# Performance work log

Hardware: AMD Instinct MI355X
Metric: run time of the kernel (lower is better)

The kernel has to match this reference:

```python
import jax, jax.numpy as jnp
import numpy as np

N = 500_000
N_ATOMS = 5
T = 8                # angle triplets per (residue, bead) table row
CONT_LEN = 36
GATE_OFFSET = 1
NUM_EXPERTS = 18
BEAD_COL = 36
MAX_BEADS = 4
ANGLE_WEIGHT = 1.0
EPS = 1e-8
MIN_LEN = 0.02


def setup_inputs() -> dict:
    key = jax.random.key(0)
    ks = jax.random.split(key, 8)
    x = jax.random.uniform(ks[0], (N, 38), dtype=jnp.float32)
    # gate column holds residue id in [1, num_experts]; bead column in [0, max_beads)
    res = jax.random.randint(ks[1], (N,), 1, NUM_EXPERTS + 1).astype(jnp.float32)
    bead = jax.random.randint(ks[2], (N,), 0, MAX_BEADS).astype(jnp.float32)
    x = x.at[:, CONT_LEN + 1].set(res)
    x = x.at[:, BEAD_COL].set(bead)
    y_true = jax.random.normal(ks[3], (N, N_ATOMS * 3), dtype=jnp.float32)
    y_pred = jax.random.normal(ks[4], (N, N_ATOMS * 3), dtype=jnp.float32)
    mask = (jax.random.uniform(ks[5], (N, N_ATOMS * 3)) < 0.85).astype(jnp.float32)
    # -1 entries act as invalid-triplet sentinels (trip_ok branch)
    trip = jax.random.randint(ks[6], (NUM_EXPERTS, MAX_BEADS, T, 3), -1, N_ATOMS, dtype=jnp.int32)
    valid = jax.random.randint(ks[7], (NUM_EXPERTS, MAX_BEADS, T), 0, 2, dtype=jnp.int32)
    return {"x": x, "y_true": y_true, "y_pred": y_pred, "mask": mask,
            "angle_triplets_table": trip, "angle_valid_table": valid}


def _atom_mse(true, pred, m):
    # masked per-atom squared error, normalized by count of valid atoms per sample
    se_atom = jnp.sum(jnp.square(true - pred) * m, axis=-1)          # [N, A]
    atom_valid = jnp.any(m > 0.0, axis=-1).astype(se_atom.dtype)     # [N, A]
    num = jnp.sum(se_atom * atom_valid, axis=-1)
    den = jnp.sum(atom_valid, axis=-1) + EPS
    return jnp.mean(num / den)


def _angle_loss(x, true, pred, m, trip_table, valid_table):
    gate = x[:, CONT_LEN + 1]
    gate = jnp.where(jnp.isfinite(gate), gate, 0.0)
    res_id = jnp.clip(jnp.round(gate).astype(jnp.int32) - GATE_OFFSET, 0, NUM_EXPERTS - 1)
    bead = x[:, BEAD_COL]
    bead = jnp.where(jnp.isfinite(bead), bead, 0.0)
    bead_id = jnp.clip(jnp.round(bead).astype(jnp.int32), 0, MAX_BEADS - 1)

    atom_valid = jnp.any(m > 0.0, axis=-1)                           # [N, A]
    trip = trip_table[res_id, bead_id]                               # [N, T, 3]
    base_valid = valid_table[res_id, bead_id]                        # [N, T]
    trip_ok = jnp.all(trip >= 0, axis=-1)
    ts = jnp.maximum(trip, 0)
    i_idx, j_idx, k_idx = ts[..., 0], ts[..., 1], ts[..., 2]         # [N, T]

    rows = jnp.arange(true.shape[0])[:, None]
    vi = atom_valid[rows, i_idx]
    vj = atom_valid[rows, j_idx]
    vk = atom_valid[rows, k_idx]
    ti, tj, tk = true[rows, i_idx], true[rows, j_idx], true[rows, k_idx]   # [N, T, 3]
    pi, pj, pk = pred[rows, i_idx], pred[rows, j_idx], pred[rows, k_idx]

    v1t, v2t, v1p, v2p = ti - tj, tk - tj, pi - pj, pk - pj
    ml2 = jnp.float32(MIN_LEN * MIN_LEN)
    sq = lambda v: jnp.sum(jnp.square(v), axis=-1)
    l1t2, l2t2, l1p2, l2p2 = sq(v1t), sq(v2t), sq(v1p), sq(v2p)

    valid = (trip_ok & (base_valid > 0) & vi & vj & vk
             & (l1t2 > ml2) & (l2t2 > ml2) & (l1p2 > ml2) & (l2p2 > ml2))

    unit = lambda v, l2: v * jax.lax.rsqrt(jnp.maximum(l2, ml2))[..., None]
    u1t, u2t = unit(v1t, l1t2), unit(v2t, l2t2)
    u1p, u2p = unit(v1p, l1p2), unit(v2p, l2p2)

    clip = lambda c: jnp.clip(c, -1.0 + 1e-6, 1.0 - 1e-6)
    cos_t = clip(jnp.sum(u1t * u2t, axis=-1))
    cos_p = clip(jnp.sum(u1p * u2p, axis=-1))
    sin_t = jnp.linalg.norm(jnp.cross(u1t, u2t), axis=-1)
    sin_p = jnp.linalg.norm(jnp.cross(u1p, u2p), axis=-1)

    per_ang = jnp.square(cos_p - cos_t) + jnp.square(sin_p - sin_t)
    per_ang = jnp.where(valid, per_ang, 0.0)
    num = jnp.sum(per_ang, axis=-1)
    den = jnp.sum(valid.astype(jnp.float32), axis=-1) + EPS
    return jnp.mean(num / den)


def reference(x, y_true, y_pred, mask, angle_triplets_table, angle_valid_table):
    true = y_true.reshape(-1, N_ATOMS, 3).astype(jnp.float32)
    pred = y_pred.reshape(-1, N_ATOMS, 3).astype(jnp.float32)
    m = mask.reshape(-1, N_ATOMS, 3).astype(jnp.float32)
    atom = _atom_mse(true, pred, m)
    ang = _angle_loss(x, true, pred, m, angle_triplets_table, angle_valid_table)
    return atom + ANGLE_WEIGHT * ang
```

## Files before the change

kernel.cpp:

```cpp
#include <hip/hip_runtime.h>
#include <math.h>

#define NEXP 18
#define NBEAD 4
#define EPSV 1e-8f
#define ML2 (0.02f * 0.02f)

#define AS1U(p) ((const __attribute__((address_space(1))) unsigned*)(p))
#define AS3U(p) ((__attribute__((address_space(3))) unsigned*)(p))

__global__ __launch_bounds__(256, 5) void loss_kernel(
    const float* __restrict__ xin, const float* __restrict__ y_true,
    const float* __restrict__ y_pred, const float* __restrict__ mask,
    const int* __restrict__ trip, const int* __restrict__ valid,
    float* __restrict__ partial, int n) {
    __shared__ float sT[3840];
    __shared__ float sP[3840];
    __shared__ unsigned sBits[124];
    __shared__ unsigned sTbl[72][4];

    const int tid = threadIdx.x;
    const int lane = tid & 63;
    const int wv = tid >> 6;

    if (tid < 124) sBits[tid] = 0u;
    if (tid < NEXP * NBEAD) {
        unsigned w[4] = {0u, 0u, 0u, 0u};
#pragma unroll
        for (int t = 0; t < 8; t++) {
            int b = tid * 8 + t;
            int i = trip[b * 3 + 0], j = trip[b * 3 + 1], k = trip[b * 3 + 2];
            unsigned ok = (i >= 0 && j >= 0 && k >= 0 && valid[b] > 0) ? 1u : 0u;
            unsigned oi = 3u * (unsigned)min(max(i, 0), 4);
            unsigned oj = 3u * (unsigned)min(max(j, 0), 4);
            unsigned ov = 3u * (unsigned)min(max(k, 0), 4);
            unsigned e = oi | (oj << 4) | (ov << 8) | (ok << 12);
            w[t >> 1] |= e << ((t & 1) * 16);
        }
        sTbl[tid][0] = w[0]; sTbl[tid][1] = w[1];
        sTbl[tid][2] = w[2]; sTbl[tid][3] = w[3];
    }
    __syncthreads();

    const int row0 = blockIdx.x * 256;
    int rows = n - row0;
    if (rows > 256) rows = 256;
    const int cnt = rows * 15;
    const int cnt4 = cnt >> 2;
    const size_t base = (size_t)row0 * 15;
    const float4* gt = (const float4*)(y_true + base);
    const float4* gp = (const float4*)(y_pred + base);
    const float4* gm = (const float4*)(mask + base);
    float4* sT4 = (float4*)sT;
    float4* sP4 = (float4*)sP;

    for (int ib = wv * 64; ib + 64 <= cnt4; ib += 256) {
        __builtin_amdgcn_global_load_lds(AS1U(gt + ib + lane), AS3U(sT4 + ib), 16, 0, 0);
        __builtin_amdgcn_global_load_lds(AS1U(gp + ib + lane), AS3U(sP4 + ib), 16, 0, 0);
    }
    for (int i = (cnt4 & ~63) + tid; i < cnt4; i += 256) { sT4[i] = gt[i]; sP4[i] = gp[i]; }
    for (int i = (cnt4 << 2) + tid; i < cnt; i += 256) {
        sT[i] = y_true[base + i];
        sP[i] = y_pred[base + i];
    }

    for (int i = tid; i < cnt4; i += 256) {
        float4 m4 = gm[i];
        unsigned b0 = (m4.x > 0.f ? 1u : 0u) | (m4.y > 0.f ? 2u : 0u) |
                      (m4.z > 0.f ? 4u : 0u) | (m4.w > 0.f ? 8u : 0u);
        if (b0) {
            int e = i << 2;
            unsigned long long v = (unsigned long long)b0 << (e & 31);
            atomicOr(&sBits[e >> 5], (unsigned)v);
            unsigned hi = (unsigned)(v >> 32);
            if (hi) atomicOr(&sBits[(e >> 5) + 1], hi);
        }
    }
    for (int i = (cnt4 << 2) + tid; i < cnt; i += 256) {
        if (mask[base + i] > 0.f) atomicOr(&sBits[i >> 5], 1u << (i & 31));
    }
    __syncthreads();

    float result = 0.0f;
    const int row = row0 + tid;
    if (row < n) {
        const float* st = sT + tid * 15;
        const float* sp = sP + tid * 15;
        const int bb = tid * 15;
        unsigned long long mw =
            ((unsigned long long)sBits[(bb >> 5) + 1] << 32) | sBits[bb >> 5];
        const unsigned mrow = (unsigned)((mw >> (bb & 31)) & 0x7fffu);

        float num_a = 0.f, den_a = 0.f;
        unsigned avm2 = 0u;
#pragma unroll
        for (int a = 0; a < 5; a++) {
            unsigned mb = (mrow >> (3 * a)) & 7u;
            float d0 = st[3 * a + 0] - sp[3 * a + 0];
            float d1 = st[3 * a + 1] - sp[3 * a + 1];
            float d2 = st[3 * a + 2] - sp[3 * a + 2];
            float se = (mb & 1u ? d0 * d0 : 0.f) + (mb & 2u ? d1 * d1 : 0.f) +
                       (mb & 4u ? d2 * d2 : 0.f);
            if (mb) { num_a += se; den_a += 1.f; avm2 |= 1u << (3 * a); }
        }
        result = num_a / (den_a + EPSV);

        float2 gb = *(const float2*)(xin + (size_t)row * 38 + 36);
        float beadf = isfinite(gb.x) ? gb.x : 0.f;
        float gatef = isfinite(gb.y) ? gb.y : 0.f;
        gatef = fminf(fmaxf(gatef, -1e6f), 1e6f);
        beadf = fminf(fmaxf(beadf, -1e6f), 1e6f);
        int res_id = min(max((int)rintf(gatef) - 1, 0), NEXP - 1);
        int bead_id = min(max((int)rintf(beadf), 0), NBEAD - 1);
        int combo = res_id * NBEAD + bead_id;
        unsigned tw0 = sTbl[combo][0], tw1 = sTbl[combo][1];
        unsigned tw2 = sTbl[combo][2], tw3 = sTbl[combo][3];

        float num_g = 0.f, den_g = 0.f;
#pragma unroll
        for (int t = 0; t < 8; t++) {
            unsigned wrd = (t < 2) ? tw0 : (t < 4) ? tw1 : (t < 6) ? tw2 : tw3;
            unsigned e = (wrd >> ((t & 1) * 16)) & 0xffffu;
            int oi = e & 15, oj = (e >> 4) & 15, ov = (e >> 8) & 15;
            bool wok = ((e >> 12) & 1u) != 0u;

            float tix = st[oi], tiy = st[oi + 1], tiz = st[oi + 2];
            float tjx = st[oj], tjy = st[oj + 1], tjz = st[oj + 2];
            float tkx = st[ov], tky = st[ov + 1], tkz = st[ov + 2];
            float pix = sp[oi], piy = sp[oi + 1], piz = sp[oi + 2];
            float pjx = sp[oj], pjy = sp[oj + 1], pjz = sp[oj + 2];
            float pkx = sp[ov], pky = sp[ov + 1], pkz = sp[ov + 2];

            float v1tx = tix - tjx, v1ty = tiy - tjy, v1tz = tiz - tjz;
            float v2tx = tkx - tjx, v2ty = tky - tjy, v2tz = tkz - tjz;
            float v1px = pix - pjx, v1py = piy - pjy, v1pz = piz - pjz;
            float v2px = pkx - pjx, v2py = pky - pjy, v2pz = pkz - pjz;

            float l1t = fmaf(v1tx, v1tx, fmaf(v1ty, v1ty, v1tz * v1tz));
            float l2t = fmaf(v2tx, v2tx, fmaf(v2ty, v2ty, v2tz * v2tz));
            float l1p = fmaf(v1px, v1px, fmaf(v1py, v1py, v1pz * v1pz));
            float l2p = fmaf(v2px, v2px, fmaf(v2py, v2py, v2pz * v2pz));

            bool okv = wok && ((avm2 >> oi) & 1) && ((avm2 >> oj) & 1) &&
                       ((avm2 >> ov) & 1) && (l1t > ML2) && (l2t > ML2) &&
                       (l1p > ML2) && (l2p > ML2);

            float rt = __builtin_amdgcn_rsqf(fmaxf(l1t, ML2) * fmaxf(l2t, ML2));
            float rp = __builtin_amdgcn_rsqf(fmaxf(l1p, ML2) * fmaxf(l2p, ML2));

            float dott = fmaf(v1tx, v2tx, fmaf(v1ty, v2ty, v1tz * v2tz));
            float dotp = fmaf(v1px, v2px, fmaf(v1py, v2py, v1pz * v2pz));
            float cut = dott * rt;
            float cup = dotp * rp;
            float cost = fminf(fmaxf(cut, -1.f + 1e-6f), 1.f - 1e-6f);
            float cosp = fminf(fmaxf(cup, -1.f + 1e-6f), 1.f - 1e-6f);
            float sint = __builtin_amdgcn_sqrtf(fmaxf(fmaf(-cut, cut, 1.f), 0.f));
            float sinp = __builtin_amdgcn_sqrtf(fmaxf(fmaf(-cup, cup, 1.f), 0.f));

            float dc = cosp - cost, dsn = sinp - sint;
            if (okv) { num_g += fmaf(dc, dc, dsn * dsn); den_g += 1.f; }
        }
        result += num_g / (den_g + EPSV);
    }

    __syncthreads();
#pragma unroll
    for (int off = 32; off > 0; off >>= 1)
        result += __shfl_down(result, off, 64);
    float* red = (float*)sBits;
    if (lane == 0) red[wv] = result;
    __syncthreads();
    if (tid == 0) partial[blockIdx.x] = red[0] + red[1] + red[2] + red[3];
}

__global__ __launch_bounds__(256) void reduce_kernel(const float* __restrict__ partial,
                                                     float* __restrict__ out, int nblocks,
                                                     float inv_n) {
    __shared__ float red[4];
    float s = 0.f;
    for (int i = threadIdx.x; i < nblocks; i += 256) s += partial[i];
#pragma unroll
    for (int off = 32; off > 0; off >>= 1) s += __shfl_down(s, off, 64);
    int lane = threadIdx.x & 63, wv = threadIdx.x >> 6;
    if (lane == 0) red[wv] = s;
    __syncthreads();
    if (threadIdx.x == 0) out[0] = (red[0] + red[1] + red[2] + red[3]) * inv_n;
}

extern "C" void kernel_launch(void* const* d_in, const int* in_sizes, int n_in,
                              void* d_out, int out_size, void* d_ws, size_t ws_size,
                              hipStream_t stream) {
    const float* x = (const float*)d_in[0];
    const float* y_true = (const float*)d_in[1];
    const float* y_pred = (const float*)d_in[2];
    const float* mask = (const float*)d_in[3];
    const int* trip = (const int*)d_in[4];
    const int* valid = (const int*)d_in[5];
    float* out = (float*)d_out;
    float* partial = (float*)d_ws;

    const int n = in_sizes[1] / 15;
    const int blocks = (n + 255) / 256;

    loss_kernel<<<blocks, 256, 0, stream>>>(x, y_true, y_pred, mask, trip, valid, partial, n);
    reduce_kernel<<<1, 256, 0, stream>>>(partial, out, blocks, 1.0f / (float)n);
}
```

Baseline: 191.1 us.

## Load rows directly per thread, pack triplet table in separate kernel

Drops the cooperative global-to-LDS block staging and the shared-memory mask bitfield built with atomics. Each thread now loads its own 15 true/pred/mask floats straight from global memory into registers and copies them to a private padded LDS slot for indexed gathers. Table packing moves to a one-block pre-kernel that writes to workspace, which removes the start-of-block syncs. The cost is uncoalesced per-thread strided loads (60-byte row stride) and one extra kernel launch.

```diff
diff --git a/kernel.cpp b/kernel.cpp
--- a/kernel.cpp
+++ b/kernel.cpp
@@ -1,109 +1,56 @@
 #include <hip/hip_runtime.h>
 #include <math.h>
 
+#define NATOMS 5
 #define NEXP 18
 #define NBEAD 4
 #define EPSV 1e-8f
 #define ML2 (0.02f * 0.02f)
 
-#define AS1U(p) ((const __attribute__((address_space(1))) unsigned*)(p))
-#define AS3U(p) ((__attribute__((address_space(3))) unsigned*)(p))
+__global__ void pack_tables(const int* __restrict__ trip, const int* __restrict__ valid,
+                            int4* __restrict__ ptbl) {
+    int c = blockIdx.x * blockDim.x + threadIdx.x;
+    if (c < NEXP * NBEAD) {
+        unsigned w[4] = {0u, 0u, 0u, 0u};
+#pragma unroll
+        for (int t = 0; t < 8; t++) {
+            int b = c * 8 + t;
+            int i = trip[b * 3 + 0], j = trip[b * 3 + 1], k = trip[b * 3 + 2];
+            unsigned ok = (i >= 0 && j >= 0 && k >= 0 && valid[b] > 0) ? 1u : 0u;
+            unsigned oi = 3u * (unsigned)min(max(i, 0), NATOMS - 1);
+            unsigned oj = 3u * (unsigned)min(max(j, 0), NATOMS - 1);
+            unsigned ov = 3u * (unsigned)min(max(k, 0), NATOMS - 1);
+            unsigned e = oi | (oj << 4) | (ov << 8) | (ok << 12);
+            w[t >> 1] |= e << ((t & 1) * 16);
+        }
+        ptbl[c] = make_int4((int)w[0], (int)w[1], (int)w[2], (int)w[3]);
+    }
+}
 
 __global__ __launch_bounds__(256, 5) void loss_kernel(
     const float* __restrict__ xin, const float* __restrict__ y_true,
     const float* __restrict__ y_pred, const float* __restrict__ mask,
-    const int* __restrict__ trip, const int* __restrict__ valid,
-    float* __restrict__ partial, int n) {
-    __shared__ float sT[3840];
-    __shared__ float sP[3840];
-    __shared__ unsigned sBits[124];
-    __shared__ unsigned sTbl[72][4];
+    const int4* __restrict__ ptbl, float* __restrict__ partial, int n) {
+    __shared__ float scr[8192];
 
     const int tid = threadIdx.x;
-    const int lane = tid & 63;
-    const int wv = tid >> 6;
-
-    if (tid < 124) sBits[tid] = 0u;
-    if (tid < NEXP * NBEAD) {
-        unsigned w[4] = {0u, 0u, 0u, 0u};
-#pragma unroll
-        for (int t = 0; t < 8; t++) {
-            int b = tid * 8 + t;
-            int i = trip[b * 3 + 0], j = trip[b * 3 + 1], k = trip[b * 3 + 2];
-            unsigned ok = (i >= 0 && j >= 0 && k >= 0 && valid[b] > 0) ? 1u : 0u;
-            unsigned oi = 3u * (unsigned)min(max(i, 0), 4);
-            unsigned oj = 3u * (unsigned)min(max(j, 0), 4);
-            unsigned ov = 3u * (unsigned)min(max(k, 0), 4);
-            unsigned e = oi | (oj << 4) | (ov << 8) | (ok << 12);
-            w[t >> 1] |= e << ((t & 1) * 16);
-        }
-        sTbl[tid][0] = w[0]; sTbl[tid][1] = w[1];
-        sTbl[tid][2] = w[2]; sTbl[tid][3] = w[3];
-    }
-    __syncthreads();
-
-    const int row0 = blockIdx.x * 256;
-    int rows = n - row0;
-    if (rows > 256) rows = 256;
-    const int cnt = rows * 15;
-    const int cnt4 = cnt >> 2;
-    const size_t base = (size_t)row0 * 15;
-    const float4* gt = (const float4*)(y_true + base);
-    const float4* gp = (const float4*)(y_pred + base);
-    const float4* gm = (const float4*)(mask + base);
-    float4* sT4 = (float4*)sT;
-    float4* sP4 = (float4*)sP;
-
-    for (int ib = wv * 64; ib + 64 <= cnt4; ib += 256) {
-        __builtin_amdgcn_global_load_lds(AS1U(gt + ib + lane), AS3U(sT4 + ib), 16, 0, 0);
-        __builtin_amdgcn_global_load_lds(AS1U(gp + ib + lane), AS3U(sP4 + ib), 16, 0, 0);
-    }
-    for (int i = (cnt4 & ~63) + tid; i < cnt4; i += 256) { sT4[i] = gt[i]; sP4[i] = gp[i]; }
-    for (int i = (cnt4 << 2) + tid; i < cnt; i += 256) {
-        sT[i] = y_true[base + i];
-        sP[i] = y_pred[base + i];
-    }
-
-    for (int i = tid; i < cnt4; i += 256) {
-        float4 m4 = gm[i];
-        unsigned b0 = (m4.x > 0.f ? 1u : 0u) | (m4.y > 0.f ? 2u : 0u) |
-                      (m4.z > 0.f ? 4u : 0u) | (m4.w > 0.f ? 8u : 0u);
-        if (b0) {
-            int e = i << 2;
-            unsigned long long v = (unsigned long long)b0 << (e & 31);
-            atomicOr(&sBits[e >> 5], (unsigned)v);
-            unsigned hi = (unsigned)(v >> 32);
-            if (hi) atomicOr(&sBits[(e >> 5) + 1], hi);
-        }
-    }
-    for (int i = (cnt4 << 2) + tid; i < cnt; i += 256) {
-        if (mask[base + i] > 0.f) atomicOr(&sBits[i >> 5], 1u << (i & 31));
-    }
-    __syncthreads();
+    const int row = blockIdx.x * 256 + tid;
+    float* st = scr + (tid << 5);
 
     float result = 0.0f;
-    const int row = row0 + tid;
     if (row < n) {
-        const float* st = sT + tid * 15;
-        const float* sp = sP + tid * 15;
-        const int bb = tid * 15;
-        unsigned long long mw =
-            ((unsigned long long)sBits[(bb >> 5) + 1] << 32) | sBits[bb >> 5];
-        const unsigned mrow = (unsigned)((mw >> (bb & 31)) & 0x7fffu);
+        const size_t rb = (size_t)row * 15;
+        const float* gT = y_true + rb;
+        const float* gP = y_pred + rb;
+        const float* gM = mask + rb;
 
-        float num_a = 0.f, den_a = 0.f;
-        unsigned avm2 = 0u;
+        float T[15], P[15], M[15];
 #pragma unroll
-        for (int a = 0; a < 5; a++) {
-            unsigned mb = (mrow >> (3 * a)) & 7u;
-            float d0 = st[3 * a + 0] - sp[3 * a + 0];
-            float d1 = st[3 * a + 1] - sp[3 * a + 1];
-            float d2 = st[3 * a + 2] - sp[3 * a + 2];
-            float se = (mb & 1u ? d0 * d0 : 0.f) + (mb & 2u ? d1 * d1 : 0.f) +
-                       (mb & 4u ? d2 * d2 : 0.f);
-            if (mb) { num_a += se; den_a += 1.f; avm2 |= 1u << (3 * a); }
-        }
-        result = num_a / (den_a + EPSV);
+        for (int c = 0; c < 15; c++) T[c] = gT[c];
+#pragma unroll
+        for (int c = 0; c < 15; c++) P[c] = gP[c];
+#pragma unroll
+        for (int c = 0; c < 15; c++) M[c] = gM[c];
 
         float2 gb = *(const float2*)(xin + (size_t)row * 38 + 36);
         float beadf = isfinite(gb.x) ? gb.x : 0.f;
@@ -112,9 +59,29 @@
         beadf = fminf(fmaxf(beadf, -1e6f), 1e6f);
         int res_id = min(max((int)rintf(gatef) - 1, 0), NEXP - 1);
         int bead_id = min(max((int)rintf(beadf), 0), NBEAD - 1);
-        int combo = res_id * NBEAD + bead_id;
-        unsigned tw0 = sTbl[combo][0], tw1 = sTbl[combo][1];
-        unsigned tw2 = sTbl[combo][2], tw3 = sTbl[combo][3];
+        int4 pk = ptbl[res_id * NBEAD + bead_id];
+        unsigned tw0 = (unsigned)pk.x, tw1 = (unsigned)pk.y;
+        unsigned tw2 = (unsigned)pk.z, tw3 = (unsigned)pk.w;
+
+#pragma unroll
+        for (int c = 0; c < 15; c++) st[c] = T[c];
+#pragma unroll
+        for (int c = 0; c < 15; c++) st[16 + c] = P[c];
+
+        float num_a = 0.f, den_a = 0.f;
+        unsigned avm2 = 0u;
+#pragma unroll
+        for (int a = 0; a < 5; a++) {
+            bool m0 = M[3 * a + 0] > 0.f;
+            bool m1 = M[3 * a + 1] > 0.f;
+            bool m2 = M[3 * a + 2] > 0.f;
+            float d0 = T[3 * a + 0] - P[3 * a + 0];
+            float d1 = T[3 * a + 1] - P[3 * a + 1];
+            float d2 = T[3 * a + 2] - P[3 * a + 2];
+            float se = (m0 ? d0 * d0 : 0.f) + (m1 ? d1 * d1 : 0.f) + (m2 ? d2 * d2 : 0.f);
+            if (m0 || m1 || m2) { num_a += se; den_a += 1.f; avm2 |= 1u << (3 * a); }
+        }
+        result = num_a / (den_a + EPSV);
 
         float num_g = 0.f, den_g = 0.f;
 #pragma unroll
@@ -127,9 +94,9 @@
             float tix = st[oi], tiy = st[oi + 1], tiz = st[oi + 2];
             float tjx = st[oj], tjy = st[oj + 1], tjz = st[oj + 2];
             float tkx = st[ov], tky = st[ov + 1], tkz = st[ov + 2];
-            float pix = sp[oi], piy = sp[oi + 1], piz = sp[oi + 2];
-            float pjx = sp[oj], pjy = sp[oj + 1], pjz = sp[oj + 2];
-            float pkx = sp[ov], pky = sp[ov + 1], pkz = sp[ov + 2];
+            float pix = st[16 + oi], piy = st[17 + oi], piz = st[18 + oi];
+            float pjx = st[16 + oj], pjy = st[17 + oj], pjz = st[18 + oj];
+            float pkx = st[16 + ov], pky = st[17 + ov], pkz = st[18 + ov];
 
             float v1tx = tix - tjx, v1ty = tiy - tjy, v1tz = tiz - tjz;
             float v2tx = tkx - tjx, v2ty = tky - tjy, v2tz = tkz - tjz;
@@ -163,11 +130,12 @@
         result += num_g / (den_g + EPSV);
     }
 
-    __syncthreads();
 #pragma unroll
     for (int off = 32; off > 0; off >>= 1)
         result += __shfl_down(result, off, 64);
-    float* red = (float*)sBits;
+    __syncthreads();
+    float* red = scr;
+    int lane = tid & 63, wv = tid >> 6;
     if (lane == 0) red[wv] = result;
     __syncthreads();
     if (tid == 0) partial[blockIdx.x] = red[0] + red[1] + red[2] + red[3];
@@ -197,11 +165,14 @@
     const int* trip = (const int*)d_in[4];
     const int* valid = (const int*)d_in[5];
     float* out = (float*)d_out;
-    float* partial = (float*)d_ws;
+
+    int4* ptbl = (int4*)d_ws;
+    float* partial = (float*)((char*)d_ws + 4096);
 
     const int n = in_sizes[1] / 15;
     const int blocks = (n + 255) / 256;
 
-    loss_kernel<<<blocks, 256, 0, stream>>>(x, y_true, y_pred, mask, trip, valid, partial, n);
+    pack_tables<<<1, 128, 0, stream>>>(trip, valid, ptbl);
+    loss_kernel<<<blocks, 256, 0, stream>>>(x, y_true, y_pred, mask, ptbl, partial, n);
     reduce_kernel<<<1, 256, 0, stream>>>(partial, out, blocks, 1.0f / (float)n);
 }
```

New measurement: 194.3 us. Within noise of the previous version (+1.7%).
